# Performance work log

Hardware: AMD Instinct MI355X
Metric: run time of the kernel (lower is better)

The kernel has to match this reference:

```python
import jax, jax.numpy as jnp
import numpy as np

D = 1024          # input_dim == output_dim == key_size
SLOTS = 128       # memory_slots
HID = 128         # write_heads hidden width
EPS = 1e-5        # LayerNorm eps (torch default)
WRITE_STRENGTH = 0.1


def _layernorm(x, g, b):
    mu = jnp.mean(x, axis=-1, keepdims=True)
    var = jnp.var(x, axis=-1, keepdims=True)
    return (x - mu) * jax.lax.rsqrt(var + EPS) * g + b


def setup_inputs() -> dict:
    key = jax.random.key(0)
    ks = jax.random.split(key, 12)
    B, S = 8, 4096
    xavier = float(np.sqrt(6.0 / (SLOTS + D)))
    return {
        "x": jax.random.normal(ks[0], (B, S, D), dtype=jnp.float32),
        "keys": jax.random.uniform(ks[1], (SLOTS, D), jnp.float32, -xavier, xavier),
        # original inits values to zeros but they become nonzero after writes; use small randn for a meaningful read
        "values": jax.random.normal(ks[2], (SLOTS, D), dtype=jnp.float32) * 0.02,
        "temperature": jnp.array([0.1], dtype=jnp.float32),
        "W1": jax.random.normal(ks[3], (D, HID), dtype=jnp.float32) * 0.02,
        "b1": jnp.zeros((HID,), jnp.float32),
        "W2": jax.random.normal(ks[4], (HID, SLOTS), dtype=jnp.float32) * 0.02,
        "b2": jnp.zeros((SLOTS,), jnp.float32),
        "Wf": jax.random.normal(ks[5], (2 * D, D), dtype=jnp.float32) * 0.02,
        "bf": jnp.zeros((D,), jnp.float32),
        "ln1_g": jnp.ones((D,), jnp.float32),
        "ln1_b": jnp.zeros((D,), jnp.float32),
        "Wo": jax.random.normal(ks[6], (D, D), dtype=jnp.float32) * 0.02,
        "bo": jnp.zeros((D,), jnp.float32),
        "ln2_g": jnp.ones((D,), jnp.float32),
        "ln2_b": jnp.zeros((D,), jnp.float32),
    }


def reference(x, keys, values, temperature, W1, b1, W2, b2, Wf, bf,
              ln1_g, ln1_b, Wo, bo, ln2_g, ln2_b):
    identity = x
    # proj_in is Identity since input_dim == output_dim
    q = x.reshape(-1, D)                                     # [N, D]
    # --- memory read: content-addressed softmax attention over SLOTS ---
    temp = jnp.clip(temperature, 1e-6, None)                 # clamp(min=1e-6)
    attn = jax.nn.softmax(q @ keys.T / temp, axis=-1)        # [N, SLOTS]
    mem_read = (attn @ values).reshape(x.shape)              # [B, S, D]
    # --- memory write (detached state update in the original) ---
    ww = jax.nn.sigmoid(jax.nn.gelu(q @ W1 + b1, approximate=False) @ W2 + b2)  # [N, SLOTS]
    new_values = values + WRITE_STRENGTH * (ww.T @ q)        # [SLOTS, D]
    # --- fusion + LN + Linear (+Dropout in eval mode = identity) ---
    fused = jnp.concatenate([x, mem_read], axis=-1) @ Wf + bf
    out = _layernorm(fused, ln1_g, ln1_b) @ Wo + bo
    # residual + post norm
    out = _layernorm(out + identity, ln2_g, ln2_b)
    return out, new_values
```

## Files before the change

### kernel.cpp

```cpp
#include <hip/hip_runtime.h>
#include <stdint.h>
#include <math.h>

typedef float f32x4 __attribute__((ext_vector_type(4)));
typedef __bf16 bf16x8_t __attribute__((ext_vector_type(8)));
typedef unsigned short us8 __attribute__((ext_vector_type(8)));
typedef unsigned short us4 __attribute__((ext_vector_type(4)));
typedef unsigned int u32;

__device__ __forceinline__ unsigned short f2bf(float f) {
  union { float f; uint32_t u; } v; v.f = f;
  uint32_t u = v.u;
  uint32_t r = (u + 0x7fffu + ((u >> 16) & 1u)) >> 16;
  return (unsigned short)r;
}
__device__ __forceinline__ float bf2f(unsigned short h) {
  union { uint32_t u; float f; } v; v.u = ((uint32_t)h) << 16;
  return v.f;
}
__device__ __forceinline__ f32x4 mfma16(us8 a, us8 b, f32x4 c) {
  return __builtin_amdgcn_mfma_f32_16x16x32_bf16(
      __builtin_bit_cast(bf16x8_t, a), __builtin_bit_cast(bf16x8_t, b), c, 0, 0, 0);
}
__device__ __forceinline__ void gl16(const void* g, void* l) {
  __builtin_amdgcn_global_load_lds(
      (const __attribute__((address_space(1))) u32*)g,
      (__attribute__((address_space(3))) u32*)l, 16, 0, 0);
}


__global__ __launch_bounds__(256) void k_tr(
    const float* __restrict__ src, unsigned short* __restrict__ dst,
    int R, int C, int dstride)
{
  __shared__ unsigned short X[64][68];
  int tile = blockIdx.x;
  int tpr = C >> 6;
  int tr = tile / tpr, tc = tile % tpr;
  int t = threadIdx.x;
  int r = t >> 2, c0 = (t & 3) * 16;
  const float* sp = src + (size_t)(tr * 64 + r) * C + tc * 64 + c0;
  #pragma unroll
  for (int q = 0; q < 4; ++q) {
    f32x4 v = *(const f32x4*)(sp + q * 4);
    us4 o;
    #pragma unroll
    for (int e = 0; e < 4; ++e) o[e] = f2bf(v[e]);
    *(us4*)&X[r][c0 + q * 4] = o;
  }
  __syncthreads();
  int o = t >> 2, k0 = (t & 3) * 16;
  us8 w0, w1;
  #pragma unroll
  for (int e = 0; e < 8; ++e) { w0[e] = X[k0 + e][o]; w1[e] = X[k0 + 8 + e][o]; }
  unsigned short* dp = dst + (size_t)(tc * 64 + o) * dstride + tr * 64 + k0;
  *(us8*)dp = w0;
  *(us8*)(dp + 8) = w1;
}

__global__ __launch_bounds__(256) void k_prep_small(
    const float* __restrict__ keys, const float* __restrict__ values,
    unsigned short* __restrict__ klw1, unsigned short* __restrict__ valB)
{
  int i = blockIdx.x * 256 + threadIdx.x;
  if (i < 131072) { klw1[i] = f2bf(keys[i]); return; }
  i -= 131072;
  valB[i] = f2bf(values[i]);
}

__global__ __launch_bounds__(256) void k_castx(
    const float* __restrict__ x, unsigned short* __restrict__ xcat)
{
  size_t idx = ((size_t)blockIdx.x * 256 + threadIdx.x) * 8;
  int row = (int)(idx >> 10), col = (int)(idx & 1023);
  f32x4 v0 = *(const f32x4*)(x + idx);
  f32x4 v1 = *(const f32x4*)(x + idx + 4);
  us8 o;
  #pragma unroll
  for (int e = 0; e < 4; ++e) { o[e] = f2bf(v0[e]); o[e + 4] = f2bf(v1[e]); }
  *(us8*)(xcat + (size_t)row * 1152 + col) = o;
}

template<int KTOT, int MT, int NTILES, int EPI>
__global__ __launch_bounds__(512, 2) void k_gemm(
    const unsigned short* __restrict__ A, int astride,
    const unsigned short* __restrict__ B,
    const float* __restrict__ bias,
    unsigned short* __restrict__ outB, float* __restrict__ outF,
    int ostride, int ocol,
    const float* __restrict__ resid)
{
  constexpr int NT = KTOT / 64;
  constexpr int AHW = MT * 64;
  constexpr int BUFHW = AHW + 16384;
  constexpr int AJ = MT / 64;
  constexpr int IFR = MT / 32;
  __shared__ __align__(16) unsigned short L[2 * BUFHW];

  int t = threadIdx.x;
  int bid = blockIdx.x;
  int logical;
  if (gridDim.x & 7) {
    logical = bid;
  } else {
    int cpx = gridDim.x >> 3;
    logical = (bid & 7) * cpx + (bid >> 3);
  }
  int m0 = (logical / NTILES) * MT, n0 = (logical % NTILES) * 256;

  int srow = t >> 3;
  int gslot = (t & 7) ^ (srow & 7);

  int w = t >> 6, l = t & 63, g = l >> 4, lc = l & 15;
  int wm = w >> 2, wn = w & 3;

  f32x4 acc[IFR][4] = {};

  auto stage = [&](int p, int kt) {
    int off = kt * 64 + gslot * 8;
    #pragma unroll
    for (int j = 0; j < AJ; ++j)
      gl16(A + (size_t)(m0 + j * 64 + srow) * astride + off,
           L + p * BUFHW + (j * 64 + srow) * 64 + (t & 7) * 8);
    #pragma unroll
    for (int j = 0; j < 4; ++j)
      gl16(B + (size_t)(n0 + j * 64 + srow) * KTOT + off,
           L + p * BUFHW + AHW + (j * 64 + srow) * 64 + (t & 7) * 8);
  };

  stage(0, 0);
  if (NT > 1) stage(1, 1);

  for (int kt = 0; kt < NT; ++kt) {
    int p = kt & 1;
    if (kt + 1 < NT) {
      if constexpr (AJ + 4 == 6) asm volatile("s_waitcnt vmcnt(6)" ::: "memory");
      else                       asm volatile("s_waitcnt vmcnt(8)" ::: "memory");
    } else {
      asm volatile("s_waitcnt vmcnt(0)" ::: "memory");
    }
    __builtin_amdgcn_s_barrier();

    const unsigned short* Ab = L + p * BUFHW;
    const unsigned short* Bb = L + p * BUFHW + AHW;
    #pragma unroll
    for (int ks = 0; ks < 2; ++ks) {
      us8 av[IFR], bv[4];
      #pragma unroll
      for (int i = 0; i < IFR; ++i) {
        int row = wm * (MT / 2) + i * 16 + lc;
        av[i] = *(const us8*)(Ab + row * 64 + (((ks * 4 + g) ^ (lc & 7)) * 8));
      }
      #pragma unroll
      for (int j = 0; j < 4; ++j) {
        int row = wn * 64 + j * 16 + lc;
        bv[j] = *(const us8*)(Bb + row * 64 + (((ks * 4 + g) ^ (lc & 7)) * 8));
      }
      __builtin_amdgcn_s_setprio(1);
      #pragma unroll
      for (int i = 0; i < IFR; ++i)
        #pragma unroll
        for (int j = 0; j < 4; ++j)
          acc[i][j] = mfma16(av[i], bv[j], acc[i][j]);
      __builtin_amdgcn_s_setprio(0);
    }
    __builtin_amdgcn_s_barrier();
    if (kt + 2 < NT) stage(p, kt + 2);
  }

  float bv4[4];
  if constexpr (EPI <= 1) {
    #pragma unroll
    for (int jn = 0; jn < 4; ++jn) bv4[jn] = bias[n0 + wn * 64 + jn * 16 + lc];
  }
  #pragma unroll
  for (int i = 0; i < IFR; ++i) {
    #pragma unroll
    for (int jj = 0; jj < 4; ++jj) {
      int row = m0 + wm * (MT / 2) + i * 16 + g * 4 + jj;
      #pragma unroll
      for (int jn = 0; jn < 4; ++jn) {
        int col = n0 + wn * 64 + jn * 16 + lc;
        float v = acc[i][jn][jj];
        if constexpr (EPI <= 1) v += bv4[jn];
        if constexpr (EPI == 1) v += resid[(size_t)row * 1024 + col];
        if constexpr (EPI == 4) {
          outB[(size_t)col * 1152 + 1024 + row] = f2bf(v);
        } else {
          size_t oa = (size_t)row * ostride + ocol + col;
          if constexpr (EPI == 0) outB[oa] = f2bf(v);
          else                    outF[oa] = v;
        }
      }
    }
  }
}

__global__ __launch_bounds__(256) void k_smx(
    const float* __restrict__ lg, const float* __restrict__ b1,
    const float* __restrict__ b2, const float* __restrict__ temp,
    const unsigned short* __restrict__ w2t,
    unsigned short* __restrict__ xcat, unsigned short* __restrict__ ww)
{
  __shared__ float lgs[16][260];
  __shared__ unsigned short hl[16][136];
  int t = threadIdx.x;
  int row0 = blockIdx.x * 16;

  {
    int r = t >> 4, c0 = (t & 15) * 16;
    const float* p = lg + (size_t)(row0 + r) * 256 + c0;
    #pragma unroll
    for (int q = 0; q < 4; ++q)
      *(f32x4*)&lgs[r][c0 + q * 4] = *(const f32x4*)(p + q * 4);
  }
  __syncthreads();

  {
    int r = t >> 4, sub = t & 15;
    float invt = 1.f / fmaxf(temp[0], 1e-6f);
    float vals[8]; float m = -3.4e38f;
    #pragma unroll
    for (int i = 0; i < 8; ++i) { vals[i] = lgs[r][sub * 8 + i]; m = fmaxf(m, vals[i]); }
    m = fmaxf(m, __shfl_xor(m, 1)); m = fmaxf(m, __shfl_xor(m, 2));
    m = fmaxf(m, __shfl_xor(m, 4)); m = fmaxf(m, __shfl_xor(m, 8));
    float ev[8]; float s = 0.f;
    #pragma unroll
    for (int i = 0; i < 8; ++i) { ev[i] = __expf((vals[i] - m) * invt); s += ev[i]; }
    s += __shfl_xor(s, 1); s += __shfl_xor(s, 2);
    s += __shfl_xor(s, 4); s += __shfl_xor(s, 8);
    float rinv = 1.f / s;
    us8 av;
    #pragma unroll
    for (int i = 0; i < 8; ++i) av[i] = f2bf(ev[i] * rinv);
    *(us8*)(xcat + (size_t)(row0 + r) * 1152 + 1024 + sub * 8) = av;
    #pragma unroll
    for (int i = 0; i < 8; ++i) {
      float v = lgs[r][128 + sub * 8 + i] + b1[sub * 8 + i];
      v = 0.5f * v * (1.f + erff(v * 0.70710678118654752f));
      hl[r][sub * 8 + i] = f2bf(v);
    }
  }
  __syncthreads();

  int w = t >> 6, l = t & 63, g = l >> 4, lc = l & 15;
  int q2 = w * 2;
  f32x4 acc[2] = {};
  #pragma unroll
  for (int ks = 0; ks < 4; ++ks) {
    us8 a = *(const us8*)&hl[lc][ks * 32 + g * 8];
    #pragma unroll
    for (int i = 0; i < 2; ++i) {
      us8 b = *(const us8*)(w2t + (size_t)((q2 + i) * 16 + lc) * 128 + ks * 32 + g * 8);
      acc[i] = mfma16(a, b, acc[i]);
    }
  }
  #pragma unroll
  for (int i = 0; i < 2; ++i) {
    int col = (q2 + i) * 16 + lc;
    float bb = b2[col];
    #pragma unroll
    for (int j = 0; j < 4; ++j) {
      int r = row0 + g * 4 + j;
      float v = acc[i][j] + bb;
      v = 1.f / (1.f + __expf(-v));
      ww[(size_t)r * 128 + col] = f2bf(v);
    }
  }
}

__global__ __launch_bounds__(256) void k_wv(
    const unsigned short* __restrict__ xcat, const unsigned short* __restrict__ ww,
    float* __restrict__ partials)
{
  __shared__ unsigned short wwT[128][40];
  __shared__ unsigned short xT[128][40];
  int t = threadIdx.x;
  int chunk = blockIdx.x >> 3;
  int dt0 = (blockIdx.x & 7) * 128;
  int w = t >> 6, l = t & 63, g = l >> 4, lc = l & 15;
  f32x4 acc[2][8] = {};
  int nn = t >> 3, e0 = (t & 7) * 16;

  for (int ks = 0; ks < 16; ++ks) {
    int n0 = chunk * 512 + ks * 32;
    __syncthreads();
    {
      us8 v0 = *(const us8*)(ww + (size_t)(n0 + nn) * 128 + e0);
      us8 v1 = *(const us8*)(ww + (size_t)(n0 + nn) * 128 + e0 + 8);
      #pragma unroll
      for (int i = 0; i < 8; ++i) { wwT[e0 + i][nn] = v0[i]; wwT[e0 + 8 + i][nn] = v1[i]; }
      const unsigned short* xp = xcat + (size_t)(n0 + nn) * 1152 + dt0 + e0;
      us8 x0 = *(const us8*)xp;
      us8 x1 = *(const us8*)(xp + 8);
      #pragma unroll
      for (int i = 0; i < 8; ++i) { xT[e0 + i][nn] = x0[i]; xT[e0 + 8 + i][nn] = x1[i]; }
    }
    __syncthreads();
    us8 bfr[8];
    #pragma unroll
    for (int i = 0; i < 8; ++i) bfr[i] = *(const us8*)&xT[i * 16 + lc][g * 8];
    #pragma unroll
    for (int st = 0; st < 2; ++st) {
      us8 a = *(const us8*)&wwT[(w * 2 + st) * 16 + lc][g * 8];
      #pragma unroll
      for (int i = 0; i < 8; ++i) acc[st][i] = mfma16(a, bfr[i], acc[st][i]);
    }
  }
  float* p = partials + (size_t)chunk * 131072;
  #pragma unroll
  for (int st = 0; st < 2; ++st)
    #pragma unroll
    for (int i = 0; i < 8; ++i)
      #pragma unroll
      for (int j = 0; j < 4; ++j) {
        int s = (w * 2 + st) * 16 + g * 4 + j;
        p[s * 1024 + dt0 + i * 16 + lc] = acc[st][i][j];
      }
}

__global__ __launch_bounds__(256) void k_red(
    const float* __restrict__ values, const float* __restrict__ partials,
    float* __restrict__ outv)
{
  int i = blockIdx.x * 256 + threadIdx.x;
  float s = 0.f;
  #pragma unroll
  for (int c = 0; c < 64; ++c) s += partials[(size_t)c * 131072 + i];
  outv[i] = values[i] + 0.1f * s;
}

__global__ __launch_bounds__(256) void k_ln1(
    unsigned short* __restrict__ fb,
    const float* __restrict__ g, const float* __restrict__ b)
{
  int w = threadIdx.x >> 6, l = threadIdx.x & 63;
  int row = blockIdx.x * 4 + w;
  unsigned short* p = fb + (size_t)row * 1024 + l * 16;
  us8 v0 = *(const us8*)p;
  us8 v1 = *(const us8*)(p + 8);
  float vf[16];
  float s = 0.f, sq = 0.f;
  #pragma unroll
  for (int e = 0; e < 8; ++e) { vf[e] = bf2f(v0[e]); vf[e + 8] = bf2f(v1[e]); }
  #pragma unroll
  for (int e = 0; e < 16; ++e) { s += vf[e]; sq += vf[e] * vf[e]; }
  #pragma unroll
  for (int msk = 1; msk < 64; msk <<= 1) {
    s += __shfl_xor(s, msk); sq += __shfl_xor(sq, msk);
  }
  float mu = s * (1.f / 1024.f);
  float rs = rsqrtf(sq * (1.f / 1024.f) - mu * mu + 1e-5f);
  float gv[16], bv[16];
  #pragma unroll
  for (int q = 0; q < 4; ++q) {
    *(f32x4*)&gv[q * 4] = *(const f32x4*)(g + l * 16 + q * 4);
    *(f32x4*)&bv[q * 4] = *(const f32x4*)(b + l * 16 + q * 4);
  }
  us8 o0, o1;
  #pragma unroll
  for (int e = 0; e < 8; ++e) {
    o0[e] = f2bf((vf[e] - mu) * rs * gv[e] + bv[e]);
    o1[e] = f2bf((vf[e + 8] - mu) * rs * gv[e + 8] + bv[e + 8]);
  }
  *(us8*)p = o0;
  *(us8*)(p + 8) = o1;
}

__global__ __launch_bounds__(256) void k_ln2a(
    const unsigned short* __restrict__ tp, const float* __restrict__ x,
    const float* __restrict__ g, const float* __restrict__ b,
    float* __restrict__ out)
{
  int w = threadIdx.x >> 6, l = threadIdx.x & 63;
  int row = blockIdx.x * 4 + w;
  size_t base = (size_t)row * 1024 + l * 16;
  us8 t0 = *(const us8*)(tp + base);
  us8 t1 = *(const us8*)(tp + base + 8);
  float vf[16];
  #pragma unroll
  for (int q = 0; q < 4; ++q) {
    f32x4 xv = *(const f32x4*)(x + base + q * 4);
    #pragma unroll
    for (int e = 0; e < 4; ++e) {
      int k = q * 4 + e;
      float tv = (k < 8) ? bf2f(t0[k]) : bf2f(t1[k - 8]);
      vf[k] = tv + xv[e];
    }
  }
  float s = 0.f, sq = 0.f;
  #pragma unroll
  for (int e = 0; e < 16; ++e) { s += vf[e]; sq += vf[e] * vf[e]; }
  #pragma unroll
  for (int msk = 1; msk < 64; msk <<= 1) {
    s += __shfl_xor(s, msk); sq += __shfl_xor(sq, msk);
  }
  float mu = s * (1.f / 1024.f);
  float rs = rsqrtf(sq * (1.f / 1024.f) - mu * mu + 1e-5f);
  #pragma unroll
  for (int q = 0; q < 4; ++q) {
    f32x4 gv = *(const f32x4*)(g + l * 16 + q * 4);
    f32x4 bv = *(const f32x4*)(b + l * 16 + q * 4);
    f32x4 o;
    #pragma unroll
    for (int e = 0; e < 4; ++e)
      o[e] = (vf[q * 4 + e] - mu) * rs * gv[e] + bv[e];
    *(f32x4*)(out + base + q * 4) = o;
  }
}

__global__ __launch_bounds__(256) void k_ln2b(
    float* __restrict__ out,
    const float* __restrict__ g, const float* __restrict__ b)
{
  int w = threadIdx.x >> 6, l = threadIdx.x & 63;
  int row = blockIdx.x * 4 + w;
  size_t base = (size_t)row * 1024 + l * 16;
  float vf[16];
  #pragma unroll
  for (int q = 0; q < 4; ++q)
    *(f32x4*)&vf[q * 4] = *(const f32x4*)(out + base + q * 4);
  float s = 0.f, sq = 0.f;
  #pragma unroll
  for (int e = 0; e < 16; ++e) { s += vf[e]; sq += vf[e] * vf[e]; }
  #pragma unroll
  for (int msk = 1; msk < 64; msk <<= 1) {
    s += __shfl_xor(s, msk); sq += __shfl_xor(sq, msk);
  }
  float mu = s * (1.f / 1024.f);
  float rs = rsqrtf(sq * (1.f / 1024.f) - mu * mu + 1e-5f);
  #pragma unroll
  for (int q = 0; q < 4; ++q) {
    f32x4 gv = *(const f32x4*)(g + l * 16 + q * 4);
    f32x4 bv = *(const f32x4*)(b + l * 16 + q * 4);
    f32x4 o;
    #pragma unroll
    for (int e = 0; e < 4; ++e)
      o[e] = (vf[q * 4 + e] - mu) * rs * gv[e] + bv[e];
    *(f32x4*)(out + base + q * 4) = o;
  }
}

extern "C" void kernel_launch(void* const* d_in, const int* in_sizes, int n_in,
                              void* d_out, int out_size, void* d_ws, size_t ws_size,
                              hipStream_t stream) {
  const float* x      = (const float*)d_in[0];
  const float* keys   = (const float*)d_in[1];
  const float* values = (const float*)d_in[2];
  const float* temp   = (const float*)d_in[3];
  const float* W1     = (const float*)d_in[4];
  const float* b1     = (const float*)d_in[5];
  const float* W2     = (const float*)d_in[6];
  const float* b2     = (const float*)d_in[7];
  const float* Wf     = (const float*)d_in[8];
  const float* bfp    = (const float*)d_in[9];
  const float* ln1g   = (const float*)d_in[10];
  const float* ln1b   = (const float*)d_in[11];
  const float* Wo     = (const float*)d_in[12];
  const float* bo     = (const float*)d_in[13];
  const float* ln2g   = (const float*)d_in[14];
  const float* ln2b   = (const float*)d_in[15];

  char* ws = (char*)d_ws;
  unsigned short* wfb   = (unsigned short*)(ws + 0);
  unsigned short* shW   = (unsigned short*)(ws + 2359296);
  unsigned short* klw1  = (unsigned short*)(ws + 4456448);
  unsigned short* w2t   = (unsigned short*)(ws + 4980736);
  unsigned short* valB  = (unsigned short*)(ws + 5013504);
  unsigned short* ww    = (unsigned short*)(ws + 5799936);
  float* lg             = (float*)(ws + 14188544);
  float* partials       = (float*)(ws + 14188544);
  unsigned short* fb    = (unsigned short*)(ws + 5799936);
  unsigned short* tprime = (unsigned short*)(ws + 72908800);
  bool bigws = (ws_size >= 140017664ULL);

  unsigned short* xcat  = (unsigned short*)d_out;
  float* out            = (float*)d_out;
  float* newvals        = (float*)((char*)d_out + 134217728);

  k_tr<<<256, 256, 0, stream>>>(Wf, wfb, 1024, 1024, 1152);
  k_tr<<<256, 256, 0, stream>>>(Wf + 1048576, shW, 1024, 1024, 1024);
  k_tr<<<32, 256, 0, stream>>>(W1, klw1 + 131072, 1024, 128, 1024);
  k_tr<<<4, 256, 0, stream>>>(W2, w2t, 128, 128, 128);
  k_prep_small<<<1024, 256, 0, stream>>>(keys, values, klw1, valB);
  k_castx<<<16384, 256, 0, stream>>>(x, xcat);

  k_gemm<1024, 128, 4, 4><<<4, 512, 0, stream>>>(
      valB, 1024, shW, nullptr, wfb, nullptr, 0, 0, nullptr);
  k_tr<<<256, 256, 0, stream>>>(Wo, shW, 1024, 1024, 1024);

  k_gemm<1024, 128, 1, 2><<<256, 512, 0, stream>>>(
      xcat, 1152, klw1, nullptr, nullptr, lg, 256, 0, nullptr);
  k_smx<<<2048, 256, 0, stream>>>(lg, b1, b2, temp, w2t, xcat, ww);

  k_wv<<<512, 256, 0, stream>>>(xcat, ww, partials);
  k_red<<<512, 256, 0, stream>>>(values, partials, newvals);

  k_gemm<1152, 256, 4, 0><<<512, 512, 0, stream>>>(
      xcat, 1152, wfb, bfp, fb, nullptr, 1024, 0, nullptr);
  k_ln1<<<8192, 256, 0, stream>>>(fb, ln1g, ln1b);

  if (bigws) {
    k_gemm<1024, 256, 4, 0><<<512, 512, 0, stream>>>(
        fb, 1024, shW, bo, tprime, nullptr, 1024, 0, nullptr);
    k_ln2a<<<8192, 256, 0, stream>>>(tprime, x, ln2g, ln2b, out);
  } else {
    k_gemm<1024, 256, 4, 1><<<512, 512, 0, stream>>>(
        fb, 1024, shW, bo, nullptr, out, 1024, 0, x);
    k_ln2b<<<8192, 256, 0, stream>>>(out, ln2g, ln2b);
  }
}
```

Baseline: 430.3 us.

## Split concatenated input into separate bf16 x and attn buffers, fuse residual into GEMM

Replaces the interleaved [x|attn] bf16 buffer with a dense bf16 copy of x and a separate attention buffer. The fusion GEMM now reads its A operand from two sources, switching to the second at K=1024. The residual add moves into the output GEMM epilogue using the bf16 copy of x, so the final LayerNorm no longer rereads fp32 x. The single workspace layout replaces the big/small workspace branch. The residual now goes through bf16 rounding, which risks lower accuracy.

```diff
diff --git a/kernel.cpp b/kernel.cpp
--- a/kernel.cpp
+++ b/kernel.cpp
@@ -69,26 +69,26 @@
 }
 
 __global__ __launch_bounds__(256) void k_castx(
-    const float* __restrict__ x, unsigned short* __restrict__ xcat)
+    const float* __restrict__ x, unsigned short* __restrict__ xb)
 {
   size_t idx = ((size_t)blockIdx.x * 256 + threadIdx.x) * 8;
-  int row = (int)(idx >> 10), col = (int)(idx & 1023);
   f32x4 v0 = *(const f32x4*)(x + idx);
   f32x4 v1 = *(const f32x4*)(x + idx + 4);
   us8 o;
   #pragma unroll
   for (int e = 0; e < 4; ++e) { o[e] = f2bf(v0[e]); o[e + 4] = f2bf(v1[e]); }
-  *(us8*)(xcat + (size_t)row * 1152 + col) = o;
-}
-
-template<int KTOT, int MT, int NTILES, int EPI>
+  *(us8*)(xb + idx) = o;
+}
+
+template<int KTOT, int MT, int NTILES, int EPI, int KSPLIT = KTOT>
 __global__ __launch_bounds__(512, 2) void k_gemm(
     const unsigned short* __restrict__ A, int astride,
+    const unsigned short* __restrict__ A2, int astride2,
     const unsigned short* __restrict__ B,
     const float* __restrict__ bias,
     unsigned short* __restrict__ outB, float* __restrict__ outF,
     int ostride, int ocol,
-    const float* __restrict__ resid)
+    const unsigned short* __restrict__ residB)
 {
   constexpr int NT = KTOT / 64;
   constexpr int AHW = MT * 64;
@@ -117,14 +117,20 @@
   f32x4 acc[IFR][4] = {};
 
   auto stage = [&](int p, int kt) {
-    int off = kt * 64 + gslot * 8;
+    int koff = kt * 64;
+    const unsigned short* Ap = A; int astr = astride;
+    if constexpr (KSPLIT < KTOT) {
+      if (koff >= KSPLIT) { Ap = A2; astr = astride2; koff -= KSPLIT; }
+    }
+    int offa = koff + gslot * 8;
+    int offb = kt * 64 + gslot * 8;
     #pragma unroll
     for (int j = 0; j < AJ; ++j)
-      gl16(A + (size_t)(m0 + j * 64 + srow) * astride + off,
+      gl16(Ap + (size_t)(m0 + j * 64 + srow) * astr + offa,
            L + p * BUFHW + (j * 64 + srow) * 64 + (t & 7) * 8);
     #pragma unroll
     for (int j = 0; j < 4; ++j)
-      gl16(B + (size_t)(n0 + j * 64 + srow) * KTOT + off,
+      gl16(B + (size_t)(n0 + j * 64 + srow) * KTOT + offb,
            L + p * BUFHW + AHW + (j * 64 + srow) * 64 + (t & 7) * 8);
   };
 
@@ -169,7 +175,7 @@
   }
 
   float bv4[4];
-  if constexpr (EPI <= 1) {
+  if constexpr (EPI == 0 || EPI == 5) {
     #pragma unroll
     for (int jn = 0; jn < 4; ++jn) bv4[jn] = bias[n0 + wn * 64 + jn * 16 + lc];
   }
@@ -182,14 +188,14 @@
       for (int jn = 0; jn < 4; ++jn) {
         int col = n0 + wn * 64 + jn * 16 + lc;
         float v = acc[i][jn][jj];
-        if constexpr (EPI <= 1) v += bv4[jn];
-        if constexpr (EPI == 1) v += resid[(size_t)row * 1024 + col];
+        if constexpr (EPI == 0 || EPI == 5) v += bv4[jn];
+        if constexpr (EPI == 5) v += bf2f(residB[(size_t)row * 1024 + col]);
         if constexpr (EPI == 4) {
           outB[(size_t)col * 1152 + 1024 + row] = f2bf(v);
         } else {
           size_t oa = (size_t)row * ostride + ocol + col;
-          if constexpr (EPI == 0) outB[oa] = f2bf(v);
-          else                    outF[oa] = v;
+          if constexpr (EPI == 0 || EPI == 5) outB[oa] = f2bf(v);
+          else                                outF[oa] = v;
         }
       }
     }
@@ -200,7 +206,7 @@
     const float* __restrict__ lg, const float* __restrict__ b1,
     const float* __restrict__ b2, const float* __restrict__ temp,
     const unsigned short* __restrict__ w2t,
-    unsigned short* __restrict__ xcat, unsigned short* __restrict__ ww)
+    unsigned short* __restrict__ attn, unsigned short* __restrict__ ww)
 {
   __shared__ float lgs[16][260];
   __shared__ unsigned short hl[16][136];
@@ -233,7 +239,7 @@
     us8 av;
     #pragma unroll
     for (int i = 0; i < 8; ++i) av[i] = f2bf(ev[i] * rinv);
-    *(us8*)(xcat + (size_t)(row0 + r) * 1152 + 1024 + sub * 8) = av;
+    *(us8*)(attn + (size_t)(row0 + r) * 128 + sub * 8) = av;
     #pragma unroll
     for (int i = 0; i < 8; ++i) {
       float v = lgs[r][128 + sub * 8 + i] + b1[sub * 8 + i];
@@ -270,7 +276,7 @@
 }
 
 __global__ __launch_bounds__(256) void k_wv(
-    const unsigned short* __restrict__ xcat, const unsigned short* __restrict__ ww,
+    const unsigned short* __restrict__ xb, const unsigned short* __restrict__ ww,
     float* __restrict__ partials)
 {
   __shared__ unsigned short wwT[128][40];
@@ -290,7 +296,7 @@
       us8 v1 = *(const us8*)(ww + (size_t)(n0 + nn) * 128 + e0 + 8);
       #pragma unroll
       for (int i = 0; i < 8; ++i) { wwT[e0 + i][nn] = v0[i]; wwT[e0 + 8 + i][nn] = v1[i]; }
-      const unsigned short* xp = xcat + (size_t)(n0 + nn) * 1152 + dt0 + e0;
+      const unsigned short* xp = xb + (size_t)(n0 + nn) * 1024 + dt0 + e0;
       us8 x0 = *(const us8*)xp;
       us8 x1 = *(const us8*)(xp + 8);
       #pragma unroll
@@ -367,8 +373,8 @@
   *(us8*)(p + 8) = o1;
 }
 
-__global__ __launch_bounds__(256) void k_ln2a(
-    const unsigned short* __restrict__ tp, const float* __restrict__ x,
+__global__ __launch_bounds__(256) void k_ln2(
+    const unsigned short* __restrict__ tp,
     const float* __restrict__ g, const float* __restrict__ b,
     float* __restrict__ out)
 {
@@ -379,47 +385,7 @@
   us8 t1 = *(const us8*)(tp + base + 8);
   float vf[16];
   #pragma unroll
-  for (int q = 0; q < 4; ++q) {
-    f32x4 xv = *(const f32x4*)(x + base + q * 4);
-    #pragma unroll
-    for (int e = 0; e < 4; ++e) {
-      int k = q * 4 + e;
-      float tv = (k < 8) ? bf2f(t0[k]) : bf2f(t1[k - 8]);
-      vf[k] = tv + xv[e];
-    }
-  }
-  float s = 0.f, sq = 0.f;
-  #pragma unroll
-  for (int e = 0; e < 16; ++e) { s += vf[e]; sq += vf[e] * vf[e]; }
-  #pragma unroll
-  for (int msk = 1; msk < 64; msk <<= 1) {
-    s += __shfl_xor(s, msk); sq += __shfl_xor(sq, msk);
-  }
-  float mu = s * (1.f / 1024.f);
-  float rs = rsqrtf(sq * (1.f / 1024.f) - mu * mu + 1e-5f);
-  #pragma unroll
-  for (int q = 0; q < 4; ++q) {
-    f32x4 gv = *(const f32x4*)(g + l * 16 + q * 4);
-    f32x4 bv = *(const f32x4*)(b + l * 16 + q * 4);
-    f32x4 o;
-    #pragma unroll
-    for (int e = 0; e < 4; ++e)
-      o[e] = (vf[q * 4 + e] - mu) * rs * gv[e] + bv[e];
-    *(f32x4*)(out + base + q * 4) = o;
-  }
-}
-
-__global__ __launch_bounds__(256) void k_ln2b(
-    float* __restrict__ out,
-    const float* __restrict__ g, const float* __restrict__ b)
-{
-  int w = threadIdx.x >> 6, l = threadIdx.x & 63;
-  int row = blockIdx.x * 4 + w;
-  size_t base = (size_t)row * 1024 + l * 16;
-  float vf[16];
-  #pragma unroll
-  for (int q = 0; q < 4; ++q)
-    *(f32x4*)&vf[q * 4] = *(const f32x4*)(out + base + q * 4);
+  for (int e = 0; e < 8; ++e) { vf[e] = bf2f(t0[e]); vf[e + 8] = bf2f(t1[e]); }
   float s = 0.f, sq = 0.f;
   #pragma unroll
   for (int e = 0; e < 16; ++e) { s += vf[e]; sq += vf[e] * vf[e]; }
@@ -467,14 +433,14 @@
   unsigned short* klw1  = (unsigned short*)(ws + 4456448);
   unsigned short* w2t   = (unsigned short*)(ws + 4980736);
   unsigned short* valB  = (unsigned short*)(ws + 5013504);
-  unsigned short* ww    = (unsigned short*)(ws + 5799936);
-  float* lg             = (float*)(ws + 14188544);
-  float* partials       = (float*)(ws + 14188544);
-  unsigned short* fb    = (unsigned short*)(ws + 5799936);
-  unsigned short* tprime = (unsigned short*)(ws + 72908800);
-  bool bigws = (ws_size >= 140017664ULL);
-
-  unsigned short* xcat  = (unsigned short*)d_out;
+  unsigned short* attn  = (unsigned short*)(ws + 5275648);
+  unsigned short* ww    = (unsigned short*)(ws + 13664256);
+  float* lg             = (float*)(ws + 22052864);
+  float* partials       = (float*)(ws + 22052864);
+  unsigned short* tprime = (unsigned short*)(ws + 22052864);
+
+  unsigned short* fb    = (unsigned short*)d_out;
+  unsigned short* xb    = (unsigned short*)((char*)d_out + 67108864);
   float* out            = (float*)d_out;
   float* newvals        = (float*)((char*)d_out + 134217728);
 
@@ -483,30 +449,24 @@
   k_tr<<<32, 256, 0, stream>>>(W1, klw1 + 131072, 1024, 128, 1024);
   k_tr<<<4, 256, 0, stream>>>(W2, w2t, 128, 128, 128);
   k_prep_small<<<1024, 256, 0, stream>>>(keys, values, klw1, valB);
-  k_castx<<<16384, 256, 0, stream>>>(x, xcat);
+  k_castx<<<16384, 256, 0, stream>>>(x, xb);
 
   k_gemm<1024, 128, 4, 4><<<4, 512, 0, stream>>>(
-      valB, 1024, shW, nullptr, wfb, nullptr, 0, 0, nullptr);
+      valB, 1024, nullptr, 0, shW, nullptr, wfb, nullptr, 0, 0, nullptr);
   k_tr<<<256, 256, 0, stream>>>(Wo, shW, 1024, 1024, 1024);
 
   k_gemm<1024, 128, 1, 2><<<256, 512, 0, stream>>>(
-      xcat, 1152, klw1, nullptr, nullptr, lg, 256, 0, nullptr);
-  k_smx<<<2048, 256, 0, stream>>>(lg, b1, b2, temp, w2t, xcat, ww);
-
-  k_wv<<<512, 256, 0, stream>>>(xcat, ww, partials);
+      xb, 1024, nullptr, 0, klw1, nullptr, nullptr, lg, 256, 0, nullptr);
+  k_smx<<<2048, 256, 0, stream>>>(lg, b1, b2, temp, w2t, attn, ww);
+
+  k_wv<<<512, 256, 0, stream>>>(xb, ww, partials);
   k_red<<<512, 256, 0, stream>>>(values, partials, newvals);
 
-  k_gemm<1152, 256, 4, 0><<<512, 512, 0, stream>>>(
-      xcat, 1152, wfb, bfp, fb, nullptr, 1024, 0, nullptr);
+  k_gemm<1152, 256, 4, 0, 1024><<<512, 512, 0, stream>>>(
+      xb, 1024, attn, 128, wfb, bfp, fb, nullptr, 1024, 0, nullptr);
   k_ln1<<<8192, 256, 0, stream>>>(fb, ln1g, ln1b);
 
-  if (bigws) {
-    k_gemm<1024, 256, 4, 0><<<512, 512, 0, stream>>>(
-        fb, 1024, shW, bo, tprime, nullptr, 1024, 0, nullptr);
-    k_ln2a<<<8192, 256, 0, stream>>>(tprime, x, ln2g, ln2b, out);
-  } else {
-    k_gemm<1024, 256, 4, 1><<<512, 512, 0, stream>>>(
-        fb, 1024, shW, bo, nullptr, out, 1024, 0, x);
-    k_ln2b<<<8192, 256, 0, stream>>>(out, ln2g, ln2b);
-  }
-}
+  k_gemm<1024, 256, 4, 5><<<512, 512, 0, stream>>>(
+      fb, 1024, nullptr, 0, shW, bo, tprime, nullptr, 1024, 0, xb);
+  k_ln2<<<8192, 256, 0, stream>>>(tprime, ln2g, ln2b, out);
+}
```

Result: faster. 405.8 us (-5.7%).
